# Optimization experiments

Hardware: AMD Instinct MI355X
Metric: run time of the kernel (lower is better)

Reference implementation:

```python
import jax, jax.numpy as jnp
import numpy as np

UNITS, IN_DIM, CH = 256, 16, 2
R0, R1, R2 = 64, 8, 2
N = 262144


def setup_inputs() -> dict:
    key = jax.random.key(0)
    ks = jax.random.split(key, 7)
    inputs = jax.random.normal(ks[0], (N, IN_DIM), dtype=jnp.float32)
    core = jax.random.normal(ks[1], (R0, R1, R2), dtype=jnp.float32) * 0.1
    factor_0 = jax.random.normal(ks[2], (UNITS, R0), dtype=jnp.float32) * 0.1
    factor_1 = jax.random.normal(ks[3], (IN_DIM, R1), dtype=jnp.float32) * 0.1
    factor_2 = jax.random.normal(ks[4], (CH, R2), dtype=jnp.float32) * 0.1
    bias = jnp.zeros((UNITS, CH), dtype=jnp.float32)
    factor = jnp.ones((UNITS, CH), dtype=jnp.float32)
    return {"inputs": inputs, "core": core, "factor_0": factor_0,
            "factor_1": factor_1, "factor_2": factor_2, "bias": bias,
            "factor": factor}


def reference(inputs, core, factor_0, factor_1, factor_2, bias, factor):
    # Tucker reconstruction of kernel: (units, in_dim, channels)
    r0 = jnp.einsum('ijn,ki->kjn', core, factor_0)      # (units, r1, r2)
    r01 = jnp.einsum('ijn,kj->ikn', r0, factor_1)       # (units, in_dim, r2)
    kernel = jnp.einsum('ijn,kn->ijk', r01, factor_2)   # (units, in_dim, ch)
    # K.dot(inputs, kernel): contract inputs last dim with kernel dim -2
    out = jnp.einsum('bi,uic->buc', inputs, kernel)     # (N, units, ch)
    out = out + bias
    out = jnp.tanh(out) * factor
    out = jnp.sum(out, axis=-1)                          # (N, units)
    return out
```

## Files before the change

### kernel.cpp

```cpp
#include <hip/hip_runtime.h>

#define UNITS 256
#define IN_DIM 16
#define CH 2
#define R0C 64
#define R1C 8
#define R2C 2
#define NROWS 262144

#define NBLK 1024
#define K2LOG2E 2.8853900817779268f

typedef float v2f __attribute__((ext_vector_type(2)));
typedef float v4f __attribute__((ext_vector_type(4)));

#define UPACK 24
#define WS_FLOATS (UNITS * UPACK)

__device__ __forceinline__ void compute_unit_params(
    int u, const float* __restrict__ core, const float* __restrict__ f0,
    const float* __restrict__ f2, const float* __restrict__ bias,
    const float* __restrict__ fac, float wout[16], float aux[5]) {
    float r0[R1C][R2C] = {};
    #pragma unroll 8
    for (int a = 0; a < R0C; ++a) {
        float f0v = f0[u * R0C + a];
        #pragma unroll
        for (int j = 0; j < R1C; ++j)
            #pragma unroll
            for (int n = 0; n < R2C; ++n)
                r0[j][n] += f0v * core[(a * R1C + j) * R2C + n];
    }
    #pragma unroll
    for (int j = 0; j < R1C; ++j) {
        float w0 = r0[j][0] * f2[0 * R2C + 0] + r0[j][1] * f2[0 * R2C + 1];
        float w1 = r0[j][0] * f2[1 * R2C + 0] + r0[j][1] * f2[1 * R2C + 1];
        wout[j * 2 + 0] = w0 * K2LOG2E;
        wout[j * 2 + 1] = w1 * K2LOG2E;
    }
    float fc0 = fac[u * CH + 0], fc1 = fac[u * CH + 1];
    aux[0] = bias[u * CH + 0] * K2LOG2E;
    aux[1] = bias[u * CH + 1] * K2LOG2E;
    aux[2] = -2.0f * fc0;
    aux[3] = -2.0f * fc1;
    aux[4] = fc0 + fc1;
}

__global__ void wprep_kernel(const float* __restrict__ core,
                             const float* __restrict__ f0,
                             const float* __restrict__ f2,
                             const float* __restrict__ bias,
                             const float* __restrict__ fac,
                             float* __restrict__ ws) {
    int u = threadIdx.x;
    float w[16], aux[5];
    compute_unit_params(u, core, f0, f2, bias, fac, w, aux);
    float* p = ws + u * UPACK;
    #pragma unroll
    for (int k = 0; k < 16; ++k) p[k] = w[k];
    #pragma unroll
    for (int k = 0; k < 5; ++k) p[16 + k] = aux[k];
    p[21] = 0.f; p[22] = 0.f; p[23] = 0.f;
}

template <bool USE_WS>
__global__ __launch_bounds__(256) void mdense_main(
    const float* __restrict__ x,
    const float* __restrict__ f1,
    const float* __restrict__ wsbuf,
    const float* __restrict__ core, const float* __restrict__ f0,
    const float* __restrict__ f2, const float* __restrict__ bias,
    const float* __restrict__ fac,
    float* __restrict__ out)
{
    __shared__ float F1s[IN_DIM * R1C];
    const int tid = threadIdx.x;
    if (tid < 32)
        reinterpret_cast<float4*>(F1s)[tid] = reinterpret_cast<const float4*>(f1)[tid];
    __syncthreads();

    const int W = blockIdx.x * 4 + (tid >> 6);
    const int lane = tid & 63;
    const int u0 = lane * 4;

    v2f wv[4][R1C];
    v2f blv[4], mv[4];
    float gs[4];
    if (USE_WS) {
        #pragma unroll
        for (int q = 0; q < 4; ++q) {
            const float4* p4 = reinterpret_cast<const float4*>(wsbuf + (u0 + q) * UPACK);
            float4 w0 = p4[0], w1 = p4[1], w2 = p4[2], w3 = p4[3], a = p4[4];
            wv[q][0] = (v2f){w0.x, w0.y}; wv[q][1] = (v2f){w0.z, w0.w};
            wv[q][2] = (v2f){w1.x, w1.y}; wv[q][3] = (v2f){w1.z, w1.w};
            wv[q][4] = (v2f){w2.x, w2.y}; wv[q][5] = (v2f){w2.z, w2.w};
            wv[q][6] = (v2f){w3.x, w3.y}; wv[q][7] = (v2f){w3.z, w3.w};
            blv[q] = (v2f){a.x, a.y};
            mv[q]  = (v2f){a.z, a.w};
            gs[q] = wsbuf[(u0 + q) * UPACK + 20];
        }
    } else {
        for (int q = 0; q < 4; ++q) {
            float w[16], aux[5];
            compute_unit_params(u0 + q, core, f0, f2, bias, fac, w, aux);
            #pragma unroll
            for (int j = 0; j < R1C; ++j) wv[q][j] = (v2f){w[j * 2], w[j * 2 + 1]};
            blv[q] = (v2f){aux[0], aux[1]};
            mv[q]  = (v2f){aux[2], aux[3]};
            gs[q] = aux[4];
        }
    }

    const size_t rowbase = (size_t)W * 64;
    const float4* xp = reinterpret_cast<const float4*>(x + (rowbase + lane) * IN_DIM);
    float4 X0 = xp[0], X1 = xp[1], X2 = xp[2], X3 = xp[3];
    const float xs[16] = {X0.x, X0.y, X0.z, X0.w, X1.x, X1.y, X1.z, X1.w,
                          X2.x, X2.y, X2.z, X2.w, X3.x, X3.y, X3.z, X3.w};
    v2f Yv[4] = {(v2f){0.f, 0.f}, (v2f){0.f, 0.f}, (v2f){0.f, 0.f}, (v2f){0.f, 0.f}};
    #pragma unroll
    for (int i = 0; i < IN_DIM; ++i) {
        v2f xv = {xs[i], xs[i]};
        float4 ha = *reinterpret_cast<const float4*>(&F1s[i * R1C]);
        float4 hb = *reinterpret_cast<const float4*>(&F1s[i * R1C + 4]);
        Yv[0] += xv * (v2f){ha.x, ha.y};
        Yv[1] += xv * (v2f){ha.z, ha.w};
        Yv[2] += xv * (v2f){hb.x, hb.y};
        Yv[3] += xv * (v2f){hb.z, hb.w};
    }
    float yl[8] = {Yv[0][0], Yv[0][1], Yv[1][0], Yv[1][1],
                   Yv[2][0], Yv[2][1], Yv[3][0], Yv[3][1]};

    auto rowval = [&](int r) -> v4f {
        float yr[8];
        #pragma unroll
        for (int j = 0; j < R1C; ++j)
            yr[j] = __int_as_float(
                __builtin_amdgcn_readlane(__float_as_int(yl[j]), r));
        v2f acc0 = blv[0], acc1 = blv[1], acc2 = blv[2], acc3 = blv[3];
        #pragma unroll
        for (int j = 0; j < R1C; ++j) {
            v2f ys = {yr[j], yr[j]};
            acc0 += ys * wv[0][j];
            acc1 += ys * wv[1][j];
            acc2 += ys * wv[2][j];
            acc3 += ys * wv[3][j];
        }
        float e00 = __builtin_amdgcn_exp2f(acc0[0]);
        float e01 = __builtin_amdgcn_exp2f(acc0[1]);
        float e10 = __builtin_amdgcn_exp2f(acc1[0]);
        float e11 = __builtin_amdgcn_exp2f(acc1[1]);
        float e20 = __builtin_amdgcn_exp2f(acc2[0]);
        float e21 = __builtin_amdgcn_exp2f(acc2[1]);
        float e30 = __builtin_amdgcn_exp2f(acc3[0]);
        float e31 = __builtin_amdgcn_exp2f(acc3[1]);
        float r00 = __builtin_amdgcn_rcpf(1.0f + e00);
        float r01 = __builtin_amdgcn_rcpf(1.0f + e01);
        float r10 = __builtin_amdgcn_rcpf(1.0f + e10);
        float r11 = __builtin_amdgcn_rcpf(1.0f + e11);
        float r20 = __builtin_amdgcn_rcpf(1.0f + e20);
        float r21 = __builtin_amdgcn_rcpf(1.0f + e21);
        float r30 = __builtin_amdgcn_rcpf(1.0f + e30);
        float r31 = __builtin_amdgcn_rcpf(1.0f + e31);
        v4f o;
        o.x = __builtin_fmaf(mv[0][0], r00, __builtin_fmaf(mv[0][1], r01, gs[0]));
        o.y = __builtin_fmaf(mv[1][0], r10, __builtin_fmaf(mv[1][1], r11, gs[1]));
        o.z = __builtin_fmaf(mv[2][0], r20, __builtin_fmaf(mv[2][1], r21, gs[2]));
        o.w = __builtin_fmaf(mv[3][0], r30, __builtin_fmaf(mv[3][1], r31, gs[3]));
        return o;
    };

    float* obase = out + rowbase * UNITS;
    for (int g2 = 0; g2 < 4; ++g2) {
        const int base = g2 * 16;
        v4f bufA[8], bufB[8];
        #pragma unroll
        for (int s = 0; s < 8; ++s) bufA[s] = rowval(base + s);
        #pragma unroll
        for (int s = 0; s < 8; ++s) {
            v4f* p4 = reinterpret_cast<v4f*>(obase + (size_t)(base + s) * UNITS) + lane;
            __builtin_nontemporal_store(bufA[s], p4);
        }
        #pragma unroll
        for (int s = 0; s < 8; ++s) bufB[s] = rowval(base + 8 + s);
        #pragma unroll
        for (int s = 0; s < 8; ++s) {
            v4f* p4 = reinterpret_cast<v4f*>(obase + (size_t)(base + 8 + s) * UNITS) + lane;
            __builtin_nontemporal_store(bufB[s], p4);
        }
    }
}

extern "C" void kernel_launch(void* const* d_in, const int* in_sizes, int n_in,
                              void* d_out, int out_size, void* d_ws, size_t ws_size,
                              hipStream_t stream) {
    const float* x    = (const float*)d_in[0];
    const float* core = (const float*)d_in[1];
    const float* f0   = (const float*)d_in[2];
    const float* f1   = (const float*)d_in[3];
    const float* f2   = (const float*)d_in[4];
    const float* bias = (const float*)d_in[5];
    const float* fac  = (const float*)d_in[6];
    float* out = (float*)d_out;

    if (ws_size >= WS_FLOATS * sizeof(float)) {
        float* ws = (float*)d_ws;
        wprep_kernel<<<1, 256, 0, stream>>>(core, f0, f2, bias, fac, ws);
        mdense_main<true><<<NBLK, 256, 0, stream>>>(x, f1, ws, core, f0, f2,
                                                    bias, fac, out);
    } else {
        mdense_main<false><<<NBLK, 256, 0, stream>>>(x, f1, nullptr, core, f0,
                                                     f2, bias, fac, out);
    }
}
```

Measured before the change: 68.68 us.

## Split into projection prep kernel and strided row-sweep output kernel

Computes the per-row rank-8 projection of the inputs in a separate prep kernel that writes it to workspace, and folds the per-unit weight prep into that kernel's first block. The main kernel then reads the projections back with a two-deep prefetch instead of using readlane broadcasts. Each wave now writes rows strided across the whole output, using normal stores instead of nontemporal ones. This adds an 8 MB workspace round trip and needs a much larger workspace; if the workspace is too small, it falls back to a single-kernel path. The prep kernel's block 0 writes the weights with no sync against other blocks, but ordering between the two launches on the same stream covers this.

Measured after the change: 104.2 us. 51.7% more time.

```diff
diff --git a/kernel.cpp b/kernel.cpp
--- a/kernel.cpp
+++ b/kernel.cpp
@@ -9,13 +9,15 @@
 #define NROWS 262144
 
 #define NBLK 1024
+#define NWAVES 4096
 #define K2LOG2E 2.8853900817779268f
 
 typedef float v2f __attribute__((ext_vector_type(2)));
 typedef float v4f __attribute__((ext_vector_type(4)));
 
 #define UPACK 24
-#define WS_FLOATS (UNITS * UPACK)
+#define YOFF 8192
+#define WS_FLOATS (YOFF + NROWS * R1C)
 
 __device__ __forceinline__ void compute_unit_params(
     int u, const float* __restrict__ core, const float* __restrict__ f0,
@@ -46,73 +48,30 @@
     aux[4] = fc0 + fc1;
 }
 
-__global__ void wprep_kernel(const float* __restrict__ core,
-                             const float* __restrict__ f0,
-                             const float* __restrict__ f2,
-                             const float* __restrict__ bias,
-                             const float* __restrict__ fac,
-                             float* __restrict__ ws) {
-    int u = threadIdx.x;
-    float w[16], aux[5];
-    compute_unit_params(u, core, f0, f2, bias, fac, w, aux);
-    float* p = ws + u * UPACK;
-    #pragma unroll
-    for (int k = 0; k < 16; ++k) p[k] = w[k];
-    #pragma unroll
-    for (int k = 0; k < 5; ++k) p[16 + k] = aux[k];
-    p[21] = 0.f; p[22] = 0.f; p[23] = 0.f;
-}
-
-template <bool USE_WS>
-__global__ __launch_bounds__(256) void mdense_main(
-    const float* __restrict__ x,
-    const float* __restrict__ f1,
-    const float* __restrict__ wsbuf,
+__global__ __launch_bounds__(256) void yprep_kernel(
+    const float* __restrict__ x, const float* __restrict__ f1,
     const float* __restrict__ core, const float* __restrict__ f0,
     const float* __restrict__ f2, const float* __restrict__ bias,
-    const float* __restrict__ fac,
-    float* __restrict__ out)
-{
+    const float* __restrict__ fac, float* __restrict__ ws) {
     __shared__ float F1s[IN_DIM * R1C];
     const int tid = threadIdx.x;
     if (tid < 32)
         reinterpret_cast<float4*>(F1s)[tid] = reinterpret_cast<const float4*>(f1)[tid];
     __syncthreads();
 
-    const int W = blockIdx.x * 4 + (tid >> 6);
-    const int lane = tid & 63;
-    const int u0 = lane * 4;
-
-    v2f wv[4][R1C];
-    v2f blv[4], mv[4];
-    float gs[4];
-    if (USE_WS) {
-        #pragma unroll
-        for (int q = 0; q < 4; ++q) {
-            const float4* p4 = reinterpret_cast<const float4*>(wsbuf + (u0 + q) * UPACK);
-            float4 w0 = p4[0], w1 = p4[1], w2 = p4[2], w3 = p4[3], a = p4[4];
-            wv[q][0] = (v2f){w0.x, w0.y}; wv[q][1] = (v2f){w0.z, w0.w};
-            wv[q][2] = (v2f){w1.x, w1.y}; wv[q][3] = (v2f){w1.z, w1.w};
-            wv[q][4] = (v2f){w2.x, w2.y}; wv[q][5] = (v2f){w2.z, w2.w};
-            wv[q][6] = (v2f){w3.x, w3.y}; wv[q][7] = (v2f){w3.z, w3.w};
-            blv[q] = (v2f){a.x, a.y};
-            mv[q]  = (v2f){a.z, a.w};
-            gs[q] = wsbuf[(u0 + q) * UPACK + 20];
-        }
-    } else {
-        for (int q = 0; q < 4; ++q) {
-            float w[16], aux[5];
-            compute_unit_params(u0 + q, core, f0, f2, bias, fac, w, aux);
-            #pragma unroll
-            for (int j = 0; j < R1C; ++j) wv[q][j] = (v2f){w[j * 2], w[j * 2 + 1]};
-            blv[q] = (v2f){aux[0], aux[1]};
-            mv[q]  = (v2f){aux[2], aux[3]};
-            gs[q] = aux[4];
-        }
-    }
-
-    const size_t rowbase = (size_t)W * 64;
-    const float4* xp = reinterpret_cast<const float4*>(x + (rowbase + lane) * IN_DIM);
+    if (blockIdx.x == 0) {
+        float w[16], aux[5];
+        compute_unit_params(tid, core, f0, f2, bias, fac, w, aux);
+        float* p = ws + tid * UPACK;
+        #pragma unroll
+        for (int k = 0; k < 16; ++k) p[k] = w[k];
+        #pragma unroll
+        for (int k = 0; k < 5; ++k) p[16 + k] = aux[k];
+        p[21] = 0.f; p[22] = 0.f; p[23] = 0.f;
+    }
+
+    const size_t row = (size_t)blockIdx.x * 256 + tid;
+    const float4* xp = reinterpret_cast<const float4*>(x + row * IN_DIM);
     float4 X0 = xp[0], X1 = xp[1], X2 = xp[2], X3 = xp[3];
     const float xs[16] = {X0.x, X0.y, X0.z, X0.w, X1.x, X1.y, X1.z, X1.w,
                           X2.x, X2.y, X2.z, X2.w, X3.x, X3.y, X3.z, X3.w};
@@ -127,15 +86,48 @@
         Yv[2] += xv * (v2f){hb.x, hb.y};
         Yv[3] += xv * (v2f){hb.z, hb.w};
     }
-    float yl[8] = {Yv[0][0], Yv[0][1], Yv[1][0], Yv[1][1],
-                   Yv[2][0], Yv[2][1], Yv[3][0], Yv[3][1]};
-
-    auto rowval = [&](int r) -> v4f {
-        float yr[8];
-        #pragma unroll
-        for (int j = 0; j < R1C; ++j)
-            yr[j] = __int_as_float(
-                __builtin_amdgcn_readlane(__float_as_int(yl[j]), r));
+    v4f* yp = reinterpret_cast<v4f*>(ws + YOFF + row * R1C);
+    yp[0] = (v4f){Yv[0][0], Yv[0][1], Yv[1][0], Yv[1][1]};
+    yp[1] = (v4f){Yv[2][0], Yv[2][1], Yv[3][0], Yv[3][1]};
+}
+
+__global__ __launch_bounds__(256) void mdense_sweep(
+    const float* __restrict__ ws, float* __restrict__ out) {
+    const int tid = threadIdx.x;
+    const int W = blockIdx.x * 4 + (tid >> 6);
+    const int lane = tid & 63;
+    const int u0 = lane * 4;
+
+    v2f wv[4][R1C];
+    v2f blv[4], mv[4];
+    float gs[4];
+    #pragma unroll
+    for (int q = 0; q < 4; ++q) {
+        const float4* p4 = reinterpret_cast<const float4*>(ws + (u0 + q) * UPACK);
+        float4 w0 = p4[0], w1 = p4[1], w2 = p4[2], w3 = p4[3], a = p4[4];
+        wv[q][0] = (v2f){w0.x, w0.y}; wv[q][1] = (v2f){w0.z, w0.w};
+        wv[q][2] = (v2f){w1.x, w1.y}; wv[q][3] = (v2f){w1.z, w1.w};
+        wv[q][4] = (v2f){w2.x, w2.y}; wv[q][5] = (v2f){w2.z, w2.w};
+        wv[q][6] = (v2f){w3.x, w3.y}; wv[q][7] = (v2f){w3.z, w3.w};
+        blv[q] = (v2f){a.x, a.y};
+        mv[q]  = (v2f){a.z, a.w};
+        gs[q] = ws[(u0 + q) * UPACK + 20];
+    }
+
+    const float* yb_ = ws + YOFF;
+    v4f ya0 = *reinterpret_cast<const v4f*>(yb_ + (size_t)W * R1C);
+    v4f yb0 = *reinterpret_cast<const v4f*>(yb_ + (size_t)W * R1C + 4);
+    v4f ya1 = *reinterpret_cast<const v4f*>(yb_ + ((size_t)NWAVES + W) * R1C);
+    v4f yb1 = *reinterpret_cast<const v4f*>(yb_ + ((size_t)NWAVES + W) * R1C + 4);
+
+    for (int k = 0; k < 64; ++k) {
+        v4f na, nb;
+        if (k < 62) {
+            const size_t rn = (size_t)(k + 2) * NWAVES + W;
+            na = *reinterpret_cast<const v4f*>(yb_ + rn * R1C);
+            nb = *reinterpret_cast<const v4f*>(yb_ + rn * R1C + 4);
+        }
+        const float yr[8] = {ya0.x, ya0.y, ya0.z, ya0.w, yb0.x, yb0.y, yb0.z, yb0.w};
         v2f acc0 = blv[0], acc1 = blv[1], acc2 = blv[2], acc3 = blv[3];
         #pragma unroll
         for (int j = 0; j < R1C; ++j) {
@@ -166,27 +158,102 @@
         o.y = __builtin_fmaf(mv[1][0], r10, __builtin_fmaf(mv[1][1], r11, gs[1]));
         o.z = __builtin_fmaf(mv[2][0], r20, __builtin_fmaf(mv[2][1], r21, gs[2]));
         o.w = __builtin_fmaf(mv[3][0], r30, __builtin_fmaf(mv[3][1], r31, gs[3]));
-        return o;
-    };
+
+        const size_t row = (size_t)k * NWAVES + W;
+        *(reinterpret_cast<v4f*>(out + row * UNITS) + lane) = o;
+
+        ya0 = ya1; yb0 = yb1;
+        ya1 = na;  yb1 = nb;
+    }
+}
+
+__global__ __launch_bounds__(256) void mdense_single(
+    const float* __restrict__ x, const float* __restrict__ f1,
+    const float* __restrict__ core, const float* __restrict__ f0,
+    const float* __restrict__ f2, const float* __restrict__ bias,
+    const float* __restrict__ fac, float* __restrict__ out) {
+    __shared__ float F1s[IN_DIM * R1C];
+    const int tid = threadIdx.x;
+    if (tid < 32)
+        reinterpret_cast<float4*>(F1s)[tid] = reinterpret_cast<const float4*>(f1)[tid];
+    __syncthreads();
+
+    const int W = blockIdx.x * 4 + (tid >> 6);
+    const int lane = tid & 63;
+    const int u0 = lane * 4;
+
+    v2f wv[4][R1C];
+    v2f blv[4], mv[4];
+    float gs[4];
+    for (int q = 0; q < 4; ++q) {
+        float w[16], aux[5];
+        compute_unit_params(u0 + q, core, f0, f2, bias, fac, w, aux);
+        #pragma unroll
+        for (int j = 0; j < R1C; ++j) wv[q][j] = (v2f){w[j * 2], w[j * 2 + 1]};
+        blv[q] = (v2f){aux[0], aux[1]};
+        mv[q]  = (v2f){aux[2], aux[3]};
+        gs[q] = aux[4];
+    }
+
+    const size_t rowbase = (size_t)W * 64;
+    const float4* xp = reinterpret_cast<const float4*>(x + (rowbase + lane) * IN_DIM);
+    float4 X0 = xp[0], X1 = xp[1], X2 = xp[2], X3 = xp[3];
+    const float xs[16] = {X0.x, X0.y, X0.z, X0.w, X1.x, X1.y, X1.z, X1.w,
+                          X2.x, X2.y, X2.z, X2.w, X3.x, X3.y, X3.z, X3.w};
+    v2f Yv[4] = {(v2f){0.f, 0.f}, (v2f){0.f, 0.f}, (v2f){0.f, 0.f}, (v2f){0.f, 0.f}};
+    #pragma unroll
+    for (int i = 0; i < IN_DIM; ++i) {
+        v2f xv = {xs[i], xs[i]};
+        float4 ha = *reinterpret_cast<const float4*>(&F1s[i * R1C]);
+        float4 hb = *reinterpret_cast<const float4*>(&F1s[i * R1C + 4]);
+        Yv[0] += xv * (v2f){ha.x, ha.y};
+        Yv[1] += xv * (v2f){ha.z, ha.w};
+        Yv[2] += xv * (v2f){hb.x, hb.y};
+        Yv[3] += xv * (v2f){hb.z, hb.w};
+    }
+    float yl[8] = {Yv[0][0], Yv[0][1], Yv[1][0], Yv[1][1],
+                   Yv[2][0], Yv[2][1], Yv[3][0], Yv[3][1]};
 
     float* obase = out + rowbase * UNITS;
-    for (int g2 = 0; g2 < 4; ++g2) {
-        const int base = g2 * 16;
-        v4f bufA[8], bufB[8];
-        #pragma unroll
-        for (int s = 0; s < 8; ++s) bufA[s] = rowval(base + s);
-        #pragma unroll
-        for (int s = 0; s < 8; ++s) {
-            v4f* p4 = reinterpret_cast<v4f*>(obase + (size_t)(base + s) * UNITS) + lane;
-            __builtin_nontemporal_store(bufA[s], p4);
+    #pragma unroll 2
+    for (int r = 0; r < 64; ++r) {
+        float yr[8];
+        #pragma unroll
+        for (int j = 0; j < R1C; ++j)
+            yr[j] = __int_as_float(
+                __builtin_amdgcn_readlane(__float_as_int(yl[j]), r));
+        v2f acc0 = blv[0], acc1 = blv[1], acc2 = blv[2], acc3 = blv[3];
+        #pragma unroll
+        for (int j = 0; j < R1C; ++j) {
+            v2f ys = {yr[j], yr[j]};
+            acc0 += ys * wv[0][j];
+            acc1 += ys * wv[1][j];
+            acc2 += ys * wv[2][j];
+            acc3 += ys * wv[3][j];
         }
-        #pragma unroll
-        for (int s = 0; s < 8; ++s) bufB[s] = rowval(base + 8 + s);
-        #pragma unroll
-        for (int s = 0; s < 8; ++s) {
-            v4f* p4 = reinterpret_cast<v4f*>(obase + (size_t)(base + 8 + s) * UNITS) + lane;
-            __builtin_nontemporal_store(bufB[s], p4);
-        }
+        v4f o;
+        float e00 = __builtin_amdgcn_exp2f(acc0[0]);
+        float e01 = __builtin_amdgcn_exp2f(acc0[1]);
+        float e10 = __builtin_amdgcn_exp2f(acc1[0]);
+        float e11 = __builtin_amdgcn_exp2f(acc1[1]);
+        float e20 = __builtin_amdgcn_exp2f(acc2[0]);
+        float e21 = __builtin_amdgcn_exp2f(acc2[1]);
+        float e30 = __builtin_amdgcn_exp2f(acc3[0]);
+        float e31 = __builtin_amdgcn_exp2f(acc3[1]);
+        float r00 = __builtin_amdgcn_rcpf(1.0f + e00);
+        float r01 = __builtin_amdgcn_rcpf(1.0f + e01);
+        float r10 = __builtin_amdgcn_rcpf(1.0f + e10);
+        float r11 = __builtin_amdgcn_rcpf(1.0f + e11);
+        float r20 = __builtin_amdgcn_rcpf(1.0f + e20);
+        float r21 = __builtin_amdgcn_rcpf(1.0f + e21);
+        float r30 = __builtin_amdgcn_rcpf(1.0f + e30);
+        float r31 = __builtin_amdgcn_rcpf(1.0f + e31);
+        o.x = __builtin_fmaf(mv[0][0], r00, __builtin_fmaf(mv[0][1], r01, gs[0]));
+        o.y = __builtin_fmaf(mv[1][0], r10, __builtin_fmaf(mv[1][1], r11, gs[1]));
+        o.z = __builtin_fmaf(mv[2][0], r20, __builtin_fmaf(mv[2][1], r21, gs[2]));
+        o.w = __builtin_fmaf(mv[3][0], r30, __builtin_fmaf(mv[3][1], r31, gs[3]));
+        v4f* p4 = reinterpret_cast<v4f*>(obase + (size_t)r * UNITS) + lane;
+        __builtin_nontemporal_store(o, p4);
     }
 }
 
@@ -204,11 +271,9 @@
 
     if (ws_size >= WS_FLOATS * sizeof(float)) {
         float* ws = (float*)d_ws;
-        wprep_kernel<<<1, 256, 0, stream>>>(core, f0, f2, bias, fac, ws);
-        mdense_main<true><<<NBLK, 256, 0, stream>>>(x, f1, ws, core, f0, f2,
-                                                    bias, fac, out);
+        yprep_kernel<<<NBLK, 256, 0, stream>>>(x, f1, core, f0, f2, bias, fac, ws);
+        mdense_sweep<<<NBLK, 256, 0, stream>>>(ws, out);
     } else {
-        mdense_main<false><<<NBLK, 256, 0, stream>>>(x, f1, nullptr, core, f0,
-                                                     f2, bias, fac, out);
-    }
-}
+        mdense_single<<<NBLK, 256, 0, stream>>>(x, f1, core, f0, f2, bias, fac, out);
+    }
+}
```

## Interleave block rows across waves via shared-memory Y staging

Applied to the files above, without the earlier changes.

Each block now computes the projected Y vectors for all 256 of its rows into LDS. Waves then process rows interleaved (row = k*4 + w) instead of each wave owning a contiguous 64-row slab. Per-row Y values come from double-buffered LDS broadcast reads instead of readlane. The aim is to spread output writes across the block and drop the scalar readlane traffic, at the cost of 8 KB LDS, an extra barrier, and a simple one-row-at-a-time store loop in place of the earlier 8-row batching.

New measurement: 75.83 us. 1.1x slower.

```diff
diff --git a/kernel.cpp b/kernel.cpp
--- a/kernel.cpp
+++ b/kernel.cpp
@@ -74,12 +74,13 @@
     float* __restrict__ out)
 {
     __shared__ float F1s[IN_DIM * R1C];
+    __shared__ float Ys[256 * R1C];
+
     const int tid = threadIdx.x;
     if (tid < 32)
         reinterpret_cast<float4*>(F1s)[tid] = reinterpret_cast<const float4*>(f1)[tid];
-    __syncthreads();
-
-    const int W = blockIdx.x * 4 + (tid >> 6);
+
+    const int w = tid >> 6;
     const int lane = tid & 63;
     const int u0 = lane * 4;
 
@@ -101,41 +102,55 @@
         }
     } else {
         for (int q = 0; q < 4; ++q) {
-            float w[16], aux[5];
-            compute_unit_params(u0 + q, core, f0, f2, bias, fac, w, aux);
+            float wq[16], aux[5];
+            compute_unit_params(u0 + q, core, f0, f2, bias, fac, wq, aux);
             #pragma unroll
-            for (int j = 0; j < R1C; ++j) wv[q][j] = (v2f){w[j * 2], w[j * 2 + 1]};
+            for (int j = 0; j < R1C; ++j) wv[q][j] = (v2f){wq[j * 2], wq[j * 2 + 1]};
             blv[q] = (v2f){aux[0], aux[1]};
             mv[q]  = (v2f){aux[2], aux[3]};
             gs[q] = aux[4];
         }
     }
 
-    const size_t rowbase = (size_t)W * 64;
-    const float4* xp = reinterpret_cast<const float4*>(x + (rowbase + lane) * IN_DIM);
-    float4 X0 = xp[0], X1 = xp[1], X2 = xp[2], X3 = xp[3];
-    const float xs[16] = {X0.x, X0.y, X0.z, X0.w, X1.x, X1.y, X1.z, X1.w,
-                          X2.x, X2.y, X2.z, X2.w, X3.x, X3.y, X3.z, X3.w};
-    v2f Yv[4] = {(v2f){0.f, 0.f}, (v2f){0.f, 0.f}, (v2f){0.f, 0.f}, (v2f){0.f, 0.f}};
-    #pragma unroll
-    for (int i = 0; i < IN_DIM; ++i) {
-        v2f xv = {xs[i], xs[i]};
-        float4 ha = *reinterpret_cast<const float4*>(&F1s[i * R1C]);
-        float4 hb = *reinterpret_cast<const float4*>(&F1s[i * R1C + 4]);
-        Yv[0] += xv * (v2f){ha.x, ha.y};
-        Yv[1] += xv * (v2f){ha.z, ha.w};
-        Yv[2] += xv * (v2f){hb.x, hb.y};
-        Yv[3] += xv * (v2f){hb.z, hb.w};
-    }
-    float yl[8] = {Yv[0][0], Yv[0][1], Yv[1][0], Yv[1][1],
-                   Yv[2][0], Yv[2][1], Yv[3][0], Yv[3][1]};
-
-    auto rowval = [&](int r) -> v4f {
-        float yr[8];
-        #pragma unroll
-        for (int j = 0; j < R1C; ++j)
-            yr[j] = __int_as_float(
-                __builtin_amdgcn_readlane(__float_as_int(yl[j]), r));
+    const size_t rowbase = (size_t)blockIdx.x * 256;
+    const int myrr = w * 64 + lane;
+    {
+        const float4* xp = reinterpret_cast<const float4*>(x + (rowbase + myrr) * IN_DIM);
+        float4 X0 = xp[0], X1 = xp[1], X2 = xp[2], X3 = xp[3];
+        const float xs[16] = {X0.x, X0.y, X0.z, X0.w, X1.x, X1.y, X1.z, X1.w,
+                              X2.x, X2.y, X2.z, X2.w, X3.x, X3.y, X3.z, X3.w};
+        v2f Yv[4] = {(v2f){0.f, 0.f}, (v2f){0.f, 0.f}, (v2f){0.f, 0.f}, (v2f){0.f, 0.f}};
+        __syncthreads();
+        #pragma unroll
+        for (int i = 0; i < IN_DIM; ++i) {
+            v2f xv = {xs[i], xs[i]};
+            float4 ha = *reinterpret_cast<const float4*>(&F1s[i * R1C]);
+            float4 hb = *reinterpret_cast<const float4*>(&F1s[i * R1C + 4]);
+            Yv[0] += xv * (v2f){ha.x, ha.y};
+            Yv[1] += xv * (v2f){ha.z, ha.w};
+            Yv[2] += xv * (v2f){hb.x, hb.y};
+            Yv[3] += xv * (v2f){hb.z, hb.w};
+        }
+        v4f* yp = reinterpret_cast<v4f*>(&Ys[myrr * R1C]);
+        yp[0] = (v4f){Yv[0][0], Yv[0][1], Yv[1][0], Yv[1][1]};
+        yp[1] = (v4f){Yv[2][0], Yv[2][1], Yv[3][0], Yv[3][1]};
+    }
+    __syncthreads();
+
+    v4f ya0 = *reinterpret_cast<const v4f*>(&Ys[w * R1C]);
+    v4f yb0 = *reinterpret_cast<const v4f*>(&Ys[w * R1C + 4]);
+    v4f ya1 = *reinterpret_cast<const v4f*>(&Ys[(4 + w) * R1C]);
+    v4f yb1 = *reinterpret_cast<const v4f*>(&Ys[(4 + w) * R1C + 4]);
+
+    float* obase = out + rowbase * UNITS;
+    for (int k = 0; k < 64; ++k) {
+        v4f na, nb;
+        if (k < 62) {
+            const int rn = (k + 2) * 4 + w;
+            na = *reinterpret_cast<const v4f*>(&Ys[rn * R1C]);
+            nb = *reinterpret_cast<const v4f*>(&Ys[rn * R1C + 4]);
+        }
+        const float yr[8] = {ya0.x, ya0.y, ya0.z, ya0.w, yb0.x, yb0.y, yb0.z, yb0.w};
         v2f acc0 = blv[0], acc1 = blv[1], acc2 = blv[2], acc3 = blv[3];
         #pragma unroll
         for (int j = 0; j < R1C; ++j) {
@@ -166,27 +181,13 @@
         o.y = __builtin_fmaf(mv[1][0], r10, __builtin_fmaf(mv[1][1], r11, gs[1]));
         o.z = __builtin_fmaf(mv[2][0], r20, __builtin_fmaf(mv[2][1], r21, gs[2]));
         o.w = __builtin_fmaf(mv[3][0], r30, __builtin_fmaf(mv[3][1], r31, gs[3]));
-        return o;
-    };
-
-    float* obase = out + rowbase * UNITS;
-    for (int g2 = 0; g2 < 4; ++g2) {
-        const int base = g2 * 16;
-        v4f bufA[8], bufB[8];
-        #pragma unroll
-        for (int s = 0; s < 8; ++s) bufA[s] = rowval(base + s);
-        #pragma unroll
-        for (int s = 0; s < 8; ++s) {
-            v4f* p4 = reinterpret_cast<v4f*>(obase + (size_t)(base + s) * UNITS) + lane;
-            __builtin_nontemporal_store(bufA[s], p4);
-        }
-        #pragma unroll
-        for (int s = 0; s < 8; ++s) bufB[s] = rowval(base + 8 + s);
-        #pragma unroll
-        for (int s = 0; s < 8; ++s) {
-            v4f* p4 = reinterpret_cast<v4f*>(obase + (size_t)(base + 8 + s) * UNITS) + lane;
-            __builtin_nontemporal_store(bufB[s], p4);
-        }
+
+        const int rr = k * 4 + w;
+        v4f* p4 = reinterpret_cast<v4f*>(obase + (size_t)rr * UNITS) + lane;
+        __builtin_nontemporal_store(o, p4);
+
+        ya0 = ya1; yb0 = yb1;
+        ya1 = na;  yb1 = nb;
     }
 }
 
```
